# Kernel optimization log

Measured on AMD Instinct MI355X. Metric: run time of the kernel, lower is better.

## Reference

```python
import jax, jax.numpy as jnp
import numpy as np

B, SQ, SK, D, DV = 8, 2048, 4096, 512, 256

def setup_inputs() -> dict:
    key = jax.random.key(0)
    k1, k2, k3, k4, k5 = jax.random.split(key, 5)
    X = jax.random.normal(k1, (B, SQ, D), dtype=jnp.float32)
    Y = jax.random.normal(k2, (SK, D), dtype=jnp.float32)
    Z = jax.random.normal(k3, (SK, D), dtype=jnp.float32)
    # Linear weights (torch stores [out, in]); scaled like default init
    W_k = jax.random.normal(k4, (D, D), dtype=jnp.float32) / np.sqrt(D)
    W_v = jax.random.normal(k5, (DV, D), dtype=jnp.float32) / np.sqrt(D)
    return {"X": X, "Y": Y, "Z": Z, "W_k": W_k, "W_v": W_v, "rate": 0}


def reference(X, Y, Z, W_k, W_v, rate):
    # key = W_k(Y).unsqueeze(0): [1, SK, D]; value = W_v(Z).unsqueeze(0): [1, SK, DV]
    key = (Y @ W_k.T)[None]
    value = (Z @ W_v.T)[None]
    # scores = X @ key^T / sqrt(d): [B, SQ, SK] (key batch dim broadcasts)
    scale = 1.0 / jnp.sqrt(jnp.asarray(X.shape[-1], dtype=X.dtype))
    scores = jnp.matmul(X, jnp.swapaxes(key, 1, 2)) * scale
    attn = jax.nn.softmax(scores, axis=-1)
    # dropout layers act as identity in eval mode
    out = jnp.matmul(attn, value)  # [B, SQ, DV]
    return out
```

## Files before the change

### kernel.cpp

```cpp
#include <hip/hip_runtime.h>
#include <hip/hip_bf16.h>

#define NB    8
#define SQN   2048
#define SKN   4096
#define DDIM  512
#define DVDIM 256
#define NROWS (NB*SQN)
#define SPLIT 2
#define SKH   (SKN/SPLIT)

typedef __attribute__((ext_vector_type(8))) short bf16x8;
typedef __attribute__((ext_vector_type(4))) short bf16x4;
typedef __attribute__((ext_vector_type(4))) float f32x4;

__device__ __forceinline__ short f2bf(float f) {
    unsigned u = __float_as_uint(f);
    return (short)((u + 0x7FFFu + ((u >> 16) & 1u)) >> 16);
}

__device__ __forceinline__ void gload_lds16(const void* g, void* l) {
    __builtin_amdgcn_global_load_lds(
        (const __attribute__((address_space(1))) unsigned int*)g,
        (__attribute__((address_space(3))) unsigned int*)l, 16, 0, 0);
}


__global__ __launch_bounds__(256, 2) void gemm_nt_f32_bf16_swz(
    const float* __restrict__ A, const float* __restrict__ Bm,
    unsigned short* __restrict__ C, int M, int N, int K, int mode)
{
    __shared__ short sA[64*128];
    __shared__ short sB[64*128];
    const int tid  = threadIdx.x;
    const int wave = tid >> 6;
    const int lane = tid & 63;
    const int quad = lane >> 4;
    const int l15  = lane & 15;
    const int m0 = blockIdx.x * 64;
    const int n0 = blockIdx.y * 64;

    f32x4 acc[4];
    #pragma unroll
    for (int n = 0; n < 4; ++n) { acc[n][0]=0.f; acc[n][1]=0.f; acc[n][2]=0.f; acc[n][3]=0.f; }

    for (int kc = 0; kc < K; kc += 128) {
        __syncthreads();
        #pragma unroll
        for (int it = 0; it < 8; ++it) {
            int f = it*1024 + tid*4;
            int row = f >> 7, col = f & 127;
            float4 av = *(const float4*)(A + (size_t)(m0+row)*K + kc + col);
            bf16x4 a4; a4[0]=f2bf(av.x); a4[1]=f2bf(av.y); a4[2]=f2bf(av.z); a4[3]=f2bf(av.w);
            *(bf16x4*)(sA + f) = a4;
            float4 bv = *(const float4*)(Bm + (size_t)(n0+row)*K + kc + col);
            bf16x4 b4; b4[0]=f2bf(bv.x); b4[1]=f2bf(bv.y); b4[2]=f2bf(bv.z); b4[3]=f2bf(bv.w);
            *(bf16x4*)(sB + f) = b4;
        }
        __syncthreads();
        #pragma unroll
        for (int t = 0; t < 4; ++t) {
            bf16x8 af = *(const bf16x8*)(sA + (wave*16 + l15)*128 + t*32 + quad*8);
            #pragma unroll
            for (int n = 0; n < 4; ++n) {
                bf16x8 bfr = *(const bf16x8*)(sB + (n*16 + l15)*128 + t*32 + quad*8);
                acc[n] = __builtin_amdgcn_mfma_f32_16x16x32_bf16(af, bfr, acc[n], 0, 0, 0);
            }
        }
    }
    #pragma unroll
    for (int n = 0; n < 4; ++n)
        #pragma unroll
        for (int r = 0; r < 4; ++r) {
            int m  = m0 + wave*16 + quad*4 + r;
            int nn = n0 + n*16 + l15;
            size_t idx;
            if (mode == 0) {
                idx = ((size_t)(m>>6)*4 + (nn>>7))*8192
                    + (size_t)((m&63)*16 + (((nn>>3)&15) ^ (m&15)))*8 + (nn&7);
            } else {
                idx = (size_t)(nn>>6)*16384
                    + (size_t)(m*8 + (((nn>>3)&7) ^ (m&7)))*8 + (nn&7);
            }
            C[idx] = (unsigned short)f2bf(acc[n][r]);
        }
}

__global__ __launch_bounds__(256, 2) void attn_fused(
    const float* __restrict__ X,
    const unsigned short* __restrict__ Kb,
    const unsigned short* __restrict__ Vt,
    float* __restrict__ Opart,
    float* __restrict__ Mpart,
    float* __restrict__ Lpart)
{
    __shared__ short sK[64*128];
    __shared__ short sV[256*64];
    __shared__ short sP[4*16*64];
    const int tid  = threadIdx.x;
    const int wave = tid >> 6;
    const int lane = tid & 63;
    const int quad = lane >> 4;
    const int l15  = lane & 15;
    const int l7   = lane & 7;
    const int q0   = blockIdx.x * 64;
    const int split = blockIdx.y;
    const float scale = 0.04419417382415922f;

    bf16x8 qf[16];
    {
        const float* xrow = X + (size_t)(q0 + wave*16 + l15) * DDIM;
        #pragma unroll
        for (int t = 0; t < 16; ++t) {
            float4 a = *(const float4*)(xrow + t*32 + quad*8);
            float4 b = *(const float4*)(xrow + t*32 + quad*8 + 4);
            bf16x8 q;
            q[0]=f2bf(a.x*scale); q[1]=f2bf(a.y*scale); q[2]=f2bf(a.z*scale); q[3]=f2bf(a.w*scale);
            q[4]=f2bf(b.x*scale); q[5]=f2bf(b.y*scale); q[6]=f2bf(b.z*scale); q[7]=f2bf(b.w*scale);
            qf[t] = q;
        }
    }

    f32x4 o[16];
    #pragma unroll
    for (int i = 0; i < 16; ++i) { o[i][0]=0.f; o[i][1]=0.f; o[i][2]=0.f; o[i][3]=0.f; }
    float m_r[4] = {-1e30f,-1e30f,-1e30f,-1e30f};
    float l_r[4] = {0.f,0.f,0.f,0.f};
    short* sPw = sP + wave*(16*64);

    for (int j = 0; j < SKH/64; ++j) {
        const int sk0 = split*SKH + j*64;
        const int sk_blk = sk0 >> 6;
        f32x4 s[4];
        #pragma unroll
        for (int n = 0; n < 4; ++n) { s[n][0]=0.f; s[n][1]=0.f; s[n][2]=0.f; s[n][3]=0.f; }

        #pragma unroll
        for (int c = 0; c < 4; ++c) {
            __syncthreads();
            if (c == 0) {
                const unsigned short* vbase = Vt + (size_t)sk_blk*16384;
                #pragma unroll
                for (int it = 0; it < 8; ++it)
                    gload_lds16(vbase + it*2048 + tid*8,
                                (char*)sV + it*4096 + wave*1024);
            }
            const unsigned short* kbase = Kb + ((size_t)sk_blk*4 + c)*8192;
            #pragma unroll
            for (int it = 0; it < 4; ++it)
                gload_lds16(kbase + it*2048 + tid*8,
                            (char*)sK + it*4096 + wave*1024);
            __syncthreads();
            #pragma unroll
            for (int t = 0; t < 4; ++t) {
                bf16x8 af = qf[c*4 + t];
                #pragma unroll
                for (int n = 0; n < 4; ++n) {
                    bf16x8 bfr = *(const bf16x8*)(sK + (n*16 + l15)*128
                                                  + (((t*4 + quad) ^ l15) << 3));
                    s[n] = __builtin_amdgcn_mfma_f32_16x16x32_bf16(af, bfr, s[n], 0, 0, 0);
                }
            }
        }

        float alpha[4];
        float p[4][4];
        #pragma unroll
        for (int r = 0; r < 4; ++r) {
            float v = fmaxf(fmaxf(s[0][r], s[1][r]), fmaxf(s[2][r], s[3][r]));
            v = fmaxf(v, __shfl_xor(v, 1));
            v = fmaxf(v, __shfl_xor(v, 2));
            v = fmaxf(v, __shfl_xor(v, 4));
            v = fmaxf(v, __shfl_xor(v, 8));
            float mn = fmaxf(m_r[r], v);
            alpha[r] = __expf(m_r[r] - mn);
            m_r[r] = mn;
            float sum = 0.f;
            #pragma unroll
            for (int n = 0; n < 4; ++n) {
                float pv = __expf(s[n][r] - mn);
                p[n][r] = pv;
                sum += pv;
            }
            sum += __shfl_xor(sum, 1);
            sum += __shfl_xor(sum, 2);
            sum += __shfl_xor(sum, 4);
            sum += __shfl_xor(sum, 8);
            l_r[r] = l_r[r]*alpha[r] + sum;
        }
        #pragma unroll
        for (int n2 = 0; n2 < 16; ++n2)
            #pragma unroll
            for (int r = 0; r < 4; ++r) o[n2][r] *= alpha[r];
        #pragma unroll
        for (int n = 0; n < 4; ++n)
            #pragma unroll
            for (int r = 0; r < 4; ++r) {
                int row = quad*4 + r;
                int cch = n*2 + (l15 >> 3);
                sPw[row*64 + (((cch ^ (row & 7)) << 3)) + l7] = f2bf(p[n][r]);
            }
        #pragma unroll
        for (int t2 = 0; t2 < 2; ++t2) {
            bf16x8 af = *(const bf16x8*)(sPw + l15*64
                                         + (((t2*4 + quad) ^ l7) << 3));
            #pragma unroll
            for (int n2 = 0; n2 < 16; ++n2) {
                bf16x8 bfr = *(const bf16x8*)(sV + (n2*16 + l15)*64
                                              + (((t2*4 + quad) ^ l7) << 3));
                o[n2] = __builtin_amdgcn_mfma_f32_16x16x32_bf16(af, bfr, o[n2], 0, 0, 0);
            }
        }
    }

    const size_t base = (size_t)split * NROWS;
    #pragma unroll
    for (int r = 0; r < 4; ++r) {
        int row = q0 + wave*16 + quad*4 + r;
        if (l15 == 0) { Mpart[base + row] = m_r[r]; Lpart[base + row] = l_r[r]; }
        float* orow = Opart + (base + row) * (size_t)DVDIM;
        #pragma unroll
        for (int n2 = 0; n2 < 16; ++n2)
            orow[n2*16 + l15] = o[n2][r];
    }
}

__global__ void combine_splits(
    const float* __restrict__ Opart, const float* __restrict__ Mpart,
    const float* __restrict__ Lpart, float* __restrict__ out)
{
    const int row = blockIdx.x;
    const int dv  = threadIdx.x;
    const size_t idx = (size_t)row * DVDIM + dv;
    float m0 = Mpart[row],         m1 = Mpart[NROWS + row];
    float l0 = Lpart[row],         l1 = Lpart[NROWS + row];
    float M  = fmaxf(m0, m1);
    float w0 = __expf(m0 - M), w1 = __expf(m1 - M);
    float denom = l0*w0 + l1*w1;
    float o0 = Opart[idx];
    float o1 = Opart[(size_t)NROWS*DVDIM + idx];
    out[idx] = (o0*w0 + o1*w1) / denom;
}

extern "C" void kernel_launch(void* const* d_in, const int* in_sizes, int n_in,
                              void* d_out, int out_size, void* d_ws, size_t ws_size,
                              hipStream_t stream) {
    const float* X  = (const float*)d_in[0];
    const float* Y  = (const float*)d_in[1];
    const float* Z  = (const float*)d_in[2];
    const float* Wk = (const float*)d_in[3];
    const float* Wv = (const float*)d_in[4];
    float* out = (float*)d_out;

    char* ws = (char*)d_ws;
    unsigned short* keyb = (unsigned short*)(ws);
    unsigned short* vtb  = (unsigned short*)(ws + (4u<<20));
    float* Opart = (float*)(ws + (8u<<20));
    float* Mpart = (float*)(ws + (8u<<20) + 33554432u);
    float* Lpart = (float*)(ws + (8u<<20) + 33554432u + 131072u);

    gemm_nt_f32_bf16_swz<<<dim3(SKN/64, DDIM/64), dim3(256), 0, stream>>>(
        Y, Wk, keyb, SKN, DDIM, DDIM, 0);
    gemm_nt_f32_bf16_swz<<<dim3(DVDIM/64, SKN/64), dim3(256), 0, stream>>>(
        Wv, Z, vtb, DVDIM, SKN, DDIM, 1);
    attn_fused<<<dim3(NROWS/64, SPLIT), dim3(256), 0, stream>>>(
        X, keyb, vtb, Opart, Mpart, Lpart);
    combine_splits<<<dim3(NROWS), dim3(256), 0, stream>>>(Opart, Mpart, Lpart, out);
}
```

Baseline: 311.7 us.

## Register-block two query row tiles per wave and prefetch whole K/V tiles

```diff
diff --git a/kernel.cpp b/kernel.cpp
--- a/kernel.cpp
+++ b/kernel.cpp
@@ -9,6 +9,7 @@
 #define NROWS (NB*SQN)
 #define SPLIT 2
 #define SKH   (SKN/SPLIT)
+#define NJ    (SKH/64)
 
 typedef __attribute__((ext_vector_type(8))) short bf16x8;
 typedef __attribute__((ext_vector_type(4))) short bf16x4;
@@ -86,7 +87,7 @@
         }
 }
 
-__global__ __launch_bounds__(256, 2) void attn_fused(
+__global__ __launch_bounds__(256, 1) void attn_fused(
     const float* __restrict__ X,
     const unsigned short* __restrict__ Kb,
     const unsigned short* __restrict__ Vt,
@@ -94,22 +95,24 @@
     float* __restrict__ Mpart,
     float* __restrict__ Lpart)
 {
-    __shared__ short sK[64*128];
-    __shared__ short sV[256*64];
-    __shared__ short sP[4*16*64];
+    __shared__ short sK[32768];
+    __shared__ short sV[2][16384];
+    __shared__ short sP[8192];
     const int tid  = threadIdx.x;
     const int wave = tid >> 6;
     const int lane = tid & 63;
     const int quad = lane >> 4;
     const int l15  = lane & 15;
     const int l7   = lane & 7;
-    const int q0   = blockIdx.x * 64;
     const int split = blockIdx.y;
+    const int q0   = blockIdx.x * 128 + wave * 32;
+    const int sb0  = split * NJ;
     const float scale = 0.04419417382415922f;
 
-    bf16x8 qf[16];
-    {
-        const float* xrow = X + (size_t)(q0 + wave*16 + l15) * DDIM;
+    bf16x8 qf[2][16];
+    #pragma unroll
+    for (int rh = 0; rh < 2; ++rh) {
+        const float* xrow = X + (size_t)(q0 + rh*16 + l15) * DDIM;
         #pragma unroll
         for (int t = 0; t < 16; ++t) {
             float4 a = *(const float4*)(xrow + t*32 + quad*8);
@@ -117,112 +120,139 @@
             bf16x8 q;
             q[0]=f2bf(a.x*scale); q[1]=f2bf(a.y*scale); q[2]=f2bf(a.z*scale); q[3]=f2bf(a.w*scale);
             q[4]=f2bf(b.x*scale); q[5]=f2bf(b.y*scale); q[6]=f2bf(b.z*scale); q[7]=f2bf(b.w*scale);
-            qf[t] = q;
-        }
-    }
-
-    f32x4 o[16];
-    #pragma unroll
-    for (int i = 0; i < 16; ++i) { o[i][0]=0.f; o[i][1]=0.f; o[i][2]=0.f; o[i][3]=0.f; }
-    float m_r[4] = {-1e30f,-1e30f,-1e30f,-1e30f};
-    float l_r[4] = {0.f,0.f,0.f,0.f};
-    short* sPw = sP + wave*(16*64);
-
-    for (int j = 0; j < SKH/64; ++j) {
-        const int sk0 = split*SKH + j*64;
-        const int sk_blk = sk0 >> 6;
-        f32x4 s[4];
-        #pragma unroll
-        for (int n = 0; n < 4; ++n) { s[n][0]=0.f; s[n][1]=0.f; s[n][2]=0.f; s[n][3]=0.f; }
-
-        #pragma unroll
-        for (int c = 0; c < 4; ++c) {
-            __syncthreads();
-            if (c == 0) {
-                const unsigned short* vbase = Vt + (size_t)sk_blk*16384;
-                #pragma unroll
-                for (int it = 0; it < 8; ++it)
-                    gload_lds16(vbase + it*2048 + tid*8,
-                                (char*)sV + it*4096 + wave*1024);
-            }
-            const unsigned short* kbase = Kb + ((size_t)sk_blk*4 + c)*8192;
-            #pragma unroll
-            for (int it = 0; it < 4; ++it)
-                gload_lds16(kbase + it*2048 + tid*8,
-                            (char*)sK + it*4096 + wave*1024);
-            __syncthreads();
-            #pragma unroll
-            for (int t = 0; t < 4; ++t) {
-                bf16x8 af = qf[c*4 + t];
+            qf[rh][t] = q;
+        }
+    }
+
+    f32x4 o[2][16];
+    #pragma unroll
+    for (int rh = 0; rh < 2; ++rh)
+        #pragma unroll
+        for (int i = 0; i < 16; ++i) { o[rh][i][0]=0.f; o[rh][i][1]=0.f; o[rh][i][2]=0.f; o[rh][i][3]=0.f; }
+    float m_r[2][4] = {{-1e30f,-1e30f,-1e30f,-1e30f},{-1e30f,-1e30f,-1e30f,-1e30f}};
+    float l_r[2][4] = {{0.f,0.f,0.f,0.f},{0.f,0.f,0.f,0.f}};
+    short* sPw = sP + wave*2048;
+
+    {
+        const unsigned short* kb = Kb + (size_t)sb0 * 32768;
+        #pragma unroll
+        for (int it = 0; it < 16; ++it)
+            gload_lds16(kb + it*2048 + tid*8, (char*)sK + it*4096 + wave*1024);
+        const unsigned short* vb = Vt + (size_t)sb0 * 16384;
+        #pragma unroll
+        for (int it = 0; it < 8; ++it)
+            gload_lds16(vb + it*2048 + tid*8, (char*)sV[0] + it*4096 + wave*1024);
+    }
+    __syncthreads();
+
+    for (int j = 0; j < NJ; ++j) {
+        f32x4 s[2][4];
+        #pragma unroll
+        for (int rh = 0; rh < 2; ++rh)
+            #pragma unroll
+            for (int n = 0; n < 4; ++n) { s[rh][n][0]=0.f; s[rh][n][1]=0.f; s[rh][n][2]=0.f; s[rh][n][3]=0.f; }
+        #pragma unroll
+        for (int t = 0; t < 16; ++t) {
+            const int cx = ((((t&3)*4 + quad) ^ l15) << 3);
+            const int cbase = (t>>2)*8192 + cx;
+            #pragma unroll
+            for (int n = 0; n < 4; ++n) {
+                bf16x8 bfr = *(const bf16x8*)(sK + cbase + (n*16 + l15)*128);
+                s[0][n] = __builtin_amdgcn_mfma_f32_16x16x32_bf16(qf[0][t], bfr, s[0][n], 0, 0, 0);
+                s[1][n] = __builtin_amdgcn_mfma_f32_16x16x32_bf16(qf[1][t], bfr, s[1][n], 0, 0, 0);
+            }
+        }
+
+        float alpha[2][4];
+        float p[2][4][4];
+        int need_rescale = 0;
+        #pragma unroll
+        for (int rh = 0; rh < 2; ++rh)
+            #pragma unroll
+            for (int r = 0; r < 4; ++r) {
+                float v = fmaxf(fmaxf(s[rh][0][r], s[rh][1][r]), fmaxf(s[rh][2][r], s[rh][3][r]));
+                v = fmaxf(v, __shfl_xor(v, 1));
+                v = fmaxf(v, __shfl_xor(v, 2));
+                v = fmaxf(v, __shfl_xor(v, 4));
+                v = fmaxf(v, __shfl_xor(v, 8));
+                float mn = fmaxf(m_r[rh][r], v);
+                float a  = __expf(m_r[rh][r] - mn);
+                alpha[rh][r] = a;
+                need_rescale |= (a < 1.0f);
+                m_r[rh][r] = mn;
+                float sum = 0.f;
                 #pragma unroll
                 for (int n = 0; n < 4; ++n) {
-                    bf16x8 bfr = *(const bf16x8*)(sK + (n*16 + l15)*128
-                                                  + (((t*4 + quad) ^ l15) << 3));
-                    s[n] = __builtin_amdgcn_mfma_f32_16x16x32_bf16(af, bfr, s[n], 0, 0, 0);
+                    float pv = __expf(s[rh][n][r] - mn);
+                    p[rh][n][r] = pv;
+                    sum += pv;
                 }
-            }
-        }
-
-        float alpha[4];
-        float p[4][4];
+                sum += __shfl_xor(sum, 1);
+                sum += __shfl_xor(sum, 2);
+                sum += __shfl_xor(sum, 4);
+                sum += __shfl_xor(sum, 8);
+                l_r[rh][r] = l_r[rh][r]*a + sum;
+            }
+        if (__any(need_rescale)) {
+            #pragma unroll
+            for (int rh = 0; rh < 2; ++rh)
+                #pragma unroll
+                for (int n2 = 0; n2 < 16; ++n2)
+                    #pragma unroll
+                    for (int r = 0; r < 4; ++r) o[rh][n2][r] *= alpha[rh][r];
+        }
+        #pragma unroll
+        for (int rh = 0; rh < 2; ++rh)
+            #pragma unroll
+            for (int n = 0; n < 4; ++n)
+                #pragma unroll
+                for (int r = 0; r < 4; ++r) {
+                    int row = rh*16 + quad*4 + r;
+                    int cch = n*2 + (l15 >> 3);
+                    sPw[row*64 + ((cch ^ (row & 7)) << 3) + l7] = f2bf(p[rh][n][r]);
+                }
+
+        __syncthreads();
+        if (j + 1 < NJ) {
+            const unsigned short* kb = Kb + (size_t)(sb0 + j + 1) * 32768;
+            #pragma unroll
+            for (int it = 0; it < 16; ++it)
+                gload_lds16(kb + it*2048 + tid*8, (char*)sK + it*4096 + wave*1024);
+            const unsigned short* vb = Vt + (size_t)(sb0 + j + 1) * 16384;
+            char* vdst = (char*)sV[(j + 1) & 1];
+            #pragma unroll
+            for (int it = 0; it < 8; ++it)
+                gload_lds16(vb + it*2048 + tid*8, vdst + it*4096 + wave*1024);
+        }
+
+        const short* sVp = sV[j & 1];
+        #pragma unroll
+        for (int t2 = 0; t2 < 2; ++t2) {
+            const int cx = (((t2*4 + quad) ^ l7) << 3);
+            bf16x8 a0 = *(const bf16x8*)(sPw + l15*64 + cx);
+            bf16x8 a1 = *(const bf16x8*)(sPw + (16 + l15)*64 + cx);
+            #pragma unroll
+            for (int n2 = 0; n2 < 16; ++n2) {
+                bf16x8 bfr = *(const bf16x8*)(sVp + (n2*16 + l15)*64 + cx);
+                o[0][n2] = __builtin_amdgcn_mfma_f32_16x16x32_bf16(a0, bfr, o[0][n2], 0, 0, 0);
+                o[1][n2] = __builtin_amdgcn_mfma_f32_16x16x32_bf16(a1, bfr, o[1][n2], 0, 0, 0);
+            }
+        }
+        if (j + 1 < NJ) __syncthreads();
+    }
+
+    const size_t base = (size_t)split * NROWS;
+    #pragma unroll
+    for (int rh = 0; rh < 2; ++rh)
         #pragma unroll
         for (int r = 0; r < 4; ++r) {
-            float v = fmaxf(fmaxf(s[0][r], s[1][r]), fmaxf(s[2][r], s[3][r]));
-            v = fmaxf(v, __shfl_xor(v, 1));
-            v = fmaxf(v, __shfl_xor(v, 2));
-            v = fmaxf(v, __shfl_xor(v, 4));
-            v = fmaxf(v, __shfl_xor(v, 8));
-            float mn = fmaxf(m_r[r], v);
-            alpha[r] = __expf(m_r[r] - mn);
-            m_r[r] = mn;
-            float sum = 0.f;
-            #pragma unroll
-            for (int n = 0; n < 4; ++n) {
-                float pv = __expf(s[n][r] - mn);
-                p[n][r] = pv;
-                sum += pv;
-            }
-            sum += __shfl_xor(sum, 1);
-            sum += __shfl_xor(sum, 2);
-            sum += __shfl_xor(sum, 4);
-            sum += __shfl_xor(sum, 8);
-            l_r[r] = l_r[r]*alpha[r] + sum;
-        }
-        #pragma unroll
-        for (int n2 = 0; n2 < 16; ++n2)
-            #pragma unroll
-            for (int r = 0; r < 4; ++r) o[n2][r] *= alpha[r];
-        #pragma unroll
-        for (int n = 0; n < 4; ++n)
-            #pragma unroll
-            for (int r = 0; r < 4; ++r) {
-                int row = quad*4 + r;
-                int cch = n*2 + (l15 >> 3);
-                sPw[row*64 + (((cch ^ (row & 7)) << 3)) + l7] = f2bf(p[n][r]);
-            }
-        #pragma unroll
-        for (int t2 = 0; t2 < 2; ++t2) {
-            bf16x8 af = *(const bf16x8*)(sPw + l15*64
-                                         + (((t2*4 + quad) ^ l7) << 3));
-            #pragma unroll
-            for (int n2 = 0; n2 < 16; ++n2) {
-                bf16x8 bfr = *(const bf16x8*)(sV + (n2*16 + l15)*64
-                                              + (((t2*4 + quad) ^ l7) << 3));
-                o[n2] = __builtin_amdgcn_mfma_f32_16x16x32_bf16(af, bfr, o[n2], 0, 0, 0);
-            }
-        }
-    }
-
-    const size_t base = (size_t)split * NROWS;
-    #pragma unroll
-    for (int r = 0; r < 4; ++r) {
-        int row = q0 + wave*16 + quad*4 + r;
-        if (l15 == 0) { Mpart[base + row] = m_r[r]; Lpart[base + row] = l_r[r]; }
-        float* orow = Opart + (base + row) * (size_t)DVDIM;
-        #pragma unroll
-        for (int n2 = 0; n2 < 16; ++n2)
-            orow[n2*16 + l15] = o[n2][r];
-    }
+            int row = q0 + rh*16 + quad*4 + r;
+            if (l15 == 0) { Mpart[base + row] = m_r[rh][r]; Lpart[base + row] = l_r[rh][r]; }
+            float* orow = Opart + (base + row) * (size_t)DVDIM;
+            #pragma unroll
+            for (int n2 = 0; n2 < 16; ++n2)
+                orow[n2*16 + l15] = o[rh][n2][r];
+        }
 }
 
 __global__ void combine_splits(
@@ -263,7 +293,7 @@
         Y, Wk, keyb, SKN, DDIM, DDIM, 0);
     gemm_nt_f32_bf16_swz<<<dim3(DVDIM/64, SKN/64), dim3(256), 0, stream>>>(
         Wv, Z, vtb, DVDIM, SKN, DDIM, 1);
-    attn_fused<<<dim3(NROWS/64, SPLIT), dim3(256), 0, stream>>>(
+    attn_fused<<<dim3(NROWS/128, SPLIT), dim3(256), 0, stream>>>(
         X, keyb, vtb, Opart, Mpart, Lpart);
     combine_splits<<<dim3(NROWS), dim3(256), 0, stream>>>(Opart, Mpart, Lpart, out);
 }
```

Measured after the change: 443.6 us. 42.3% more time.
